# Kernel optimization log

Hardware: AMD Instinct MI355X
Metric: run time of the kernel (lower is better)

Reference implementation:

```python
import jax, jax.numpy as jnp
import numpy as np

D, H, DK = 512, 8, 64
SCALE = 1.5 / 1.0  # gamma/tau, schedule='const'
NEG = -1e30


def _cross(x_q, x_kv, mask_kv, Wq, Wk, Wv, scale):
    # x_q: [B,Tq,D], x_kv: [B,Tk,D], mask_kv: [B,Tk] (1=keep, 0=mask)
    B, Tq, _ = x_q.shape
    Tk = x_kv.shape[1]
    q = (x_q @ Wq.T).reshape(B, Tq, H, DK).transpose(0, 2, 1, 3)
    k = (x_kv @ Wk.T).reshape(B, Tk, H, DK).transpose(0, 2, 1, 3)
    v = (x_kv @ Wv.T).reshape(B, Tk, H, DK).transpose(0, 2, 1, 3)
    logits = jnp.einsum('bhqd,bhkd->bhqk', q, k) * (scale / jnp.sqrt(jnp.float32(DK)))
    if mask_kv is not None:
        logits = jnp.where(mask_kv[:, None, None, :] == 0, NEG, logits)
    attn = jax.nn.softmax(logits, axis=-1)
    out = jnp.einsum('bhqk,bhkd->bhqd', attn, v)
    return out.transpose(0, 2, 1, 3).reshape(B, Tq, D)


def setup_inputs() -> dict:
    key = jax.random.key(0)
    ks = jax.random.split(key, 12)
    B, T = 4, 2048
    inp = {
        'skel_seq': jax.random.normal(ks[0], (B, T, D), jnp.float32),
        'sens_seq': jax.random.normal(ks[1], (B, T, D), jnp.float32),
        'mask_skel': jax.random.randint(ks[2], (B, T), 0, 2, jnp.int32),
        'mask_sens': jax.random.randint(ks[3], (B, T), 0, 2, jnp.int32),
    }
    s = 1.0 / np.sqrt(D)
    names = ['Wq_s2e', 'Wk_e', 'Wv_e', 'Wq_e2s', 'Wk_s', 'Wv_s', 'Wo_s', 'Wo_e']
    for i, n in enumerate(names):
        inp[n] = jax.random.normal(ks[4 + i], (D, D), jnp.float32) * s
    return inp


def reference(skel_seq, sens_seq, mask_skel, mask_sens,
              Wq_s2e, Wk_e, Wv_e, Wq_e2s, Wk_s, Wv_s, Wo_s, Wo_e):
    # skel queries attend over sensor keys/values
    s2e = _cross(skel_seq, sens_seq, mask_sens, Wq_s2e, Wk_e, Wv_e, SCALE) @ Wo_e.T
    # sensor queries attend over skeleton keys/values
    e2s = _cross(sens_seq, skel_seq, mask_skel, Wq_e2s, Wk_s, Wv_s, SCALE) @ Wo_s.T
    return (e2s, s2e)
```

## Files before the change

kernel.cpp:

```cpp
#include <hip/hip_runtime.h>
#include <hip/hip_bf16.h>

#define T_SEQ 2048
#define N_TOK 4194304
#define W_ELEM 262144


typedef float f32x4  __attribute__((ext_vector_type(4)));
typedef short bf16x8 __attribute__((ext_vector_type(8)));

#define SCALE_Q 0.27050532f

__device__ __forceinline__ unsigned short f2b(float f) {
    __hip_bfloat16 h = __float2bfloat16(f);
    return *reinterpret_cast<unsigned short*>(&h);
}

__device__ __forceinline__ int pack2bf(float lo, float hi) {
    return ((int)f2b(hi) << 16) | (int)f2b(lo);
}

__device__ __forceinline__ bf16x8 ldg8(const unsigned short* p) {
    union { int4 i; bf16x8 b; } u;
    u.i = *reinterpret_cast<const int4*>(p);
    return u.b;
}

__device__ __forceinline__ float fexp2(float x) {
#if __has_builtin(__builtin_amdgcn_exp2f)
    return __builtin_amdgcn_exp2f(x);
#else
    return exp2f(x);
#endif
}

typedef unsigned int u32_g __attribute__((address_space(1)));
typedef unsigned int u32_l __attribute__((address_space(3)));
__device__ __forceinline__ void gload_lds16(const void* g, void* l) {
    __builtin_amdgcn_global_load_lds((const u32_g*)g, (u32_l*)l, 16, 0, 0);
}

__device__ __forceinline__ void raw_barrier() {
    __builtin_amdgcn_sched_barrier(0);
    __builtin_amdgcn_s_barrier();
    __builtin_amdgcn_sched_barrier(0);
}

__global__ __launch_bounds__(256)
void prep_bias(const int* __restrict__ ms, const int* __restrict__ mk,
               float* __restrict__ dst)
{
    const int i = (blockIdx.x * 256 + threadIdx.x) * 8;
    const int* m = (i >> 13) ? mk : ms;
    const int rem = i & 8191;
    const int4 a = *reinterpret_cast<const int4*>(&m[rem]);
    const int4 b = *reinterpret_cast<const int4*>(&m[rem + 4]);
    float4 f0, f1;
    f0.x = a.x ? 0.0f : -3e38f; f0.y = a.y ? 0.0f : -3e38f;
    f0.z = a.z ? 0.0f : -3e38f; f0.w = a.w ? 0.0f : -3e38f;
    f1.x = b.x ? 0.0f : -3e38f; f1.y = b.y ? 0.0f : -3e38f;
    f1.z = b.z ? 0.0f : -3e38f; f1.w = b.w ? 0.0f : -3e38f;
    *reinterpret_cast<float4*>(&dst[i])     = f0;
    *reinterpret_cast<float4*>(&dst[i + 4]) = f1;
}

__global__ __launch_bounds__(256)
void to_bf16(const float* __restrict__ s0, const float* __restrict__ s1,
             const float* __restrict__ w0, const float* __restrict__ w1,
             const float* __restrict__ w2, const float* __restrict__ w3,
             const float* __restrict__ w4, const float* __restrict__ w5,
             unsigned short* __restrict__ dst)
{
    const int bid = blockIdx.x;
    int y, x;
    if (bid < 4096) { y = bid >> 11; x = bid & 2047; }
    else { const int t = bid - 4096; y = 2 + (t >> 7); x = t & 127; }
    const float* src;
    size_t off;
    switch (y) {
        case 0: src = s0; off = 0;      break;
        case 1: src = s1; off = N_TOK;  break;
        case 2: src = w0; off = 2 * (size_t)N_TOK;              break;
        case 3: src = w1; off = 2 * (size_t)N_TOK + 1 * W_ELEM; break;
        case 4: src = w2; off = 2 * (size_t)N_TOK + 2 * W_ELEM; break;
        case 5: src = w3; off = 2 * (size_t)N_TOK + 3 * W_ELEM; break;
        case 6: src = w4; off = 2 * (size_t)N_TOK + 4 * W_ELEM; break;
        default: src = w5; off = 2 * (size_t)N_TOK + 5 * W_ELEM; break;
    }
    const int idx = (x * 256 + threadIdx.x) * 8;
    const float4 a = *reinterpret_cast<const float4*>(src + idx);
    const float4 b = *reinterpret_cast<const float4*>(src + idx + 4);
    int4 o;
    o.x = pack2bf(a.x, a.y); o.y = pack2bf(a.z, a.w);
    o.z = pack2bf(b.x, b.y); o.w = pack2bf(b.z, b.w);
    *reinterpret_cast<int4*>(dst + off + idx) = o;
}

#define MF_SETUP                                                               \
    __shared__ short Asm[64][72];                                              \
    __shared__ short Wsm[64][72];                                              \
    const int tid  = threadIdx.x;                                              \
    const int lane = tid & 63;                                                 \
    const int w4   = tid >> 6;                                                 \
    const int nl   = lane & 15;                                                \
    const int quad = lane >> 4;                                                \
    const int n0 = blockIdx.x * 64;                                            \
    const int m0 = blockIdx.y * 64;                                            \
    const int arow = tid >> 2;                                                 \
    const int acol = (tid & 3) * 16;                                           \
    f32x4 acc[4] = {};

#define MF_WRITE_W                                                             \
    {                                                                          \
        int4 x;                                                                \
        x.x = pack2bf(wv[0].x, wv[0].y); x.y = pack2bf(wv[0].z, wv[0].w);      \
        x.z = pack2bf(wv[1].x, wv[1].y); x.w = pack2bf(wv[1].z, wv[1].w);      \
        *reinterpret_cast<int4*>(&Wsm[arow][acol]) = x;                        \
        x.x = pack2bf(wv[2].x, wv[2].y); x.y = pack2bf(wv[2].z, wv[2].w);      \
        x.z = pack2bf(wv[3].x, wv[3].y); x.w = pack2bf(wv[3].z, wv[3].w);      \
        *reinterpret_cast<int4*>(&Wsm[arow][acol + 8]) = x;                    \
    }

#define MF_MMA_LOOP                                                            \
    _Pragma("unroll")                                                          \
    for (int kc = 0; kc < 2; ++kc) {                                           \
        const bf16x8 a = *reinterpret_cast<const bf16x8*>(                     \
            &Asm[w4 * 16 + nl][kc * 32 + quad * 8]);                           \
        _Pragma("unroll")                                                      \
        for (int c = 0; c < 4; ++c) {                                          \
            const bf16x8 bf = *reinterpret_cast<const bf16x8*>(                \
                &Wsm[c * 16 + nl][kc * 32 + quad * 8]);                        \
            acc[c] = __builtin_amdgcn_mfma_f32_16x16x32_bf16(a, bf, acc[c],    \
                                                             0, 0, 0);         \
        }                                                                      \
    }

#define MF_CWRITE_PROJ                                                         \
    if (!trans) {                                                              \
        _Pragma("unroll")                                                      \
        for (int c = 0; c < 4; ++c)                                            \
            _Pragma("unroll")                                                  \
            for (int r = 0; r < 4; ++r)                                        \
                C[(size_t)(m0 + w4 * 16 + quad * 4 + r) * 512 + n0 + c * 16 + nl] = \
                    f2b(acc[c][r] * alpha);                                    \
    } else {                                                                   \
        const int b  = m0 >> 11;                                               \
        const int t0 = (m0 & 2047) + w4 * 16 + quad * 4;                       \
        _Pragma("unroll")                                                      \
        for (int c = 0; c < 4; ++c) {                                          \
            const int n = n0 + c * 16 + nl;                                    \
            ushort4 o;                                                         \
            o.x = f2b(acc[c][0]);                                              \
            o.y = f2b(acc[c][1]);                                              \
            o.z = f2b(acc[c][2]);                                              \
            o.w = f2b(acc[c][3]);                                              \
            *reinterpret_cast<ushort4*>(C + (size_t)(b * 512 + n) * T_SEQ + t0) = o; \
        }                                                                      \
    }

__global__ __launch_bounds__(256)
void proj_all(const float* __restrict__ skel, const float* __restrict__ sens,
              const float* __restrict__ Wq1, const float* __restrict__ Wk1,
              const float* __restrict__ Wv1, const float* __restrict__ Wq2,
              const float* __restrict__ Wk2, const float* __restrict__ Wv2,
              unsigned short* __restrict__ Q1, unsigned short* __restrict__ K1,
              unsigned short* __restrict__ Vt1, unsigned short* __restrict__ Q2,
              unsigned short* __restrict__ K2, unsigned short* __restrict__ Vt2,
              int zbase)
{
    const int z = zbase + blockIdx.z;
    const float* A; const float* W; unsigned short* C;
    float alpha = 1.0f; bool trans = false;
    switch (z) {
        case 0:  A = skel; W = Wq1; C = Q1; alpha = SCALE_Q; break;
        case 1:  A = sens; W = Wk1; C = K1; break;
        case 2:  A = sens; W = Wv1; C = Vt1; trans = true; break;
        case 3:  A = sens; W = Wq2; C = Q2; alpha = SCALE_Q; break;
        case 4:  A = skel; W = Wk2; C = K2; break;
        default: A = skel; W = Wv2; C = Vt2; trans = true; break;
    }

    MF_SETUP
    const float* ap = A + (size_t)(m0 + arow) * 512 + acol;
    const float* wp = W + (size_t)(n0 + arow) * 512 + acol;
    float4 av[4], wv[4];
    #pragma unroll
    for (int j = 0; j < 4; ++j) {
        av[j] = *reinterpret_cast<const float4*>(ap + 4 * j);
        wv[j] = *reinterpret_cast<const float4*>(wp + 4 * j);
    }
    for (int it = 0; it < 8; ++it) {
        __syncthreads();
        {
            int4 x;
            x.x = pack2bf(av[0].x, av[0].y); x.y = pack2bf(av[0].z, av[0].w);
            x.z = pack2bf(av[1].x, av[1].y); x.w = pack2bf(av[1].z, av[1].w);
            *reinterpret_cast<int4*>(&Asm[arow][acol]) = x;
            x.x = pack2bf(av[2].x, av[2].y); x.y = pack2bf(av[2].z, av[2].w);
            x.z = pack2bf(av[3].x, av[3].y); x.w = pack2bf(av[3].z, av[3].w);
            *reinterpret_cast<int4*>(&Asm[arow][acol + 8]) = x;
        }
        MF_WRITE_W
        __syncthreads();
        if (it < 7) {
            const float* apn = ap + (it + 1) * 64;
            const float* wpn = wp + (it + 1) * 64;
            #pragma unroll
            for (int j = 0; j < 4; ++j) {
                av[j] = *reinterpret_cast<const float4*>(apn + 4 * j);
                wv[j] = *reinterpret_cast<const float4*>(wpn + 4 * j);
            }
        }
        MF_MMA_LOOP
    }
    MF_CWRITE_PROJ
}

__global__ __launch_bounds__(256, 3)
void proj_fused(const unsigned short* __restrict__ skb,
                const unsigned short* __restrict__ snb,
                const unsigned short* __restrict__ wball,
                unsigned short* __restrict__ Q1, unsigned short* __restrict__ K1,
                unsigned short* __restrict__ Vt1, unsigned short* __restrict__ Q2,
                unsigned short* __restrict__ K2, unsigned short* __restrict__ Vt2)
{
    __shared__ __align__(16) char smem[49152];
    short (*Al)[128][32] = reinterpret_cast<short (*)[128][32]>(smem);
    short (*Wl)[128][32] = reinterpret_cast<short (*)[128][32]>(smem + 24576);

    const int o   = blockIdx.x;
    const int wg  = (o & 7) * 192 + (o >> 3);
    const int z   = wg >> 8;
    const int idx = wg & 255;
    const int nh  = idx & 3;
    const int mt  = idx >> 2;

    const unsigned short* A = (z == 0 || z >= 4) ? skb : snb;
    const unsigned short* W = wball + (size_t)z * W_ELEM;
    unsigned short* C;
    switch (z) {
        case 0: C = Q1;  break;
        case 1: C = K1;  break;
        case 2: C = Vt1; break;
        case 3: C = Q2;  break;
        case 4: C = K2;  break;
        default: C = Vt2; break;
    }
    const bool trans = (z == 2 || z == 5);
    const float alpha = (z == 0 || z == 3) ? SCALE_Q : 1.0f;

    const int tid  = threadIdx.x;
    const int w    = tid >> 6;
    const int wr   = w >> 1;
    const int wc   = w & 1;
    const int lane = tid & 63;
    const int nl   = lane & 15;
    const int quad = lane >> 4;
    const int rof  = lane >> 2;
    const int cg   = (lane & 3) ^ ((lane >> 3) & 3);

    const int m0g = mt * 128;
    const int n0  = nh * 128;

    const unsigned short* srcA0 = A + (size_t)(m0g + w * 32 + rof) * 512 + cg * 8;
    const unsigned short* srcA1 = srcA0 + (size_t)16 * 512;
    const unsigned short* srcW0 = W + (size_t)(n0 + w * 32 + rof) * 512 + cg * 8;
    const unsigned short* srcW1 = srcW0 + (size_t)16 * 512;

    f32x4 acc[4][4] = {};

    auto stage = [&](int it, int buf) {
        const int k0 = it * 32;
        gload_lds16(srcA0 + k0, &Al[buf][w * 32][0]);
        gload_lds16(srcA1 + k0, &Al[buf][w * 32 + 16][0]);
        gload_lds16(srcW0 + k0, &Wl[buf][w * 32][0]);
        gload_lds16(srcW1 + k0, &Wl[buf][w * 32 + 16][0]);
    };

    stage(0, 0);
    stage(1, 1);
    asm volatile("s_waitcnt vmcnt(4)" ::: "memory");
    raw_barrier();

    const int key = (nl >> 1) & 3;
    int bcur = 0, bpre = 2;
    for (int it = 0; it < 16; ++it) {
        if (it < 14) stage(it + 2, bpre);
        bf16x8 a[4], bb[4];
        #pragma unroll
        for (int am = 0; am < 4; ++am)
            a[am] = *reinterpret_cast<const bf16x8*>(
                &Al[bcur][wr * 64 + am * 16 + nl][(quad ^ key) * 8]);
        #pragma unroll
        for (int bn = 0; bn < 4; ++bn)
            bb[bn] = *reinterpret_cast<const bf16x8*>(
                &Wl[bcur][wc * 64 + bn * 16 + nl][(quad ^ key) * 8]);
        #pragma unroll
        for (int am = 0; am < 4; ++am)
            #pragma unroll
            for (int bn = 0; bn < 4; ++bn)
                acc[am][bn] = __builtin_amdgcn_mfma_f32_16x16x32_bf16(
                    a[am], bb[bn], acc[am][bn], 0, 0, 0);
        if (it < 14)       asm volatile("s_waitcnt vmcnt(4)" ::: "memory");
        else if (it == 14) asm volatile("s_waitcnt vmcnt(0)" ::: "memory");
        raw_barrier();
        bcur = (bcur == 2) ? 0 : bcur + 1;
        bpre = (bpre == 2) ? 0 : bpre + 1;
    }

    if (!trans) {
        short (*Cl)[136] = reinterpret_cast<short (*)[136]>(smem);
        #pragma unroll
        for (int am = 0; am < 4; ++am)
            #pragma unroll
            for (int bn = 0; bn < 4; ++bn)
                #pragma unroll
                for (int r = 0; r < 4; ++r)
                    Cl[wr * 64 + am * 16 + quad * 4 + r][wc * 64 + bn * 16 + nl] =
                        (short)f2b(acc[am][bn][r] * alpha);
        __syncthreads();
        const int lr = tid >> 1;
        const int ch = (tid & 1) * 64;
        unsigned short* cp = C + (size_t)(m0g + lr) * 512 + n0 + ch;
        #pragma unroll
        for (int j = 0; j < 8; ++j)
            *reinterpret_cast<int4*>(cp + j * 8) =
                *reinterpret_cast<const int4*>(&Cl[lr][ch + j * 8]);
    } else {
        short (*Tl)[136] = reinterpret_cast<short (*)[136]>(smem);
        #pragma unroll
        for (int am = 0; am < 4; ++am)
            #pragma unroll
            for (int bn = 0; bn < 4; ++bn) {
                int* dst = reinterpret_cast<int*>(
                    &Tl[wc * 64 + bn * 16 + nl][wr * 64 + am * 16 + quad * 4]);
                dst[0] = pack2bf(acc[am][bn][0], acc[am][bn][1]);
                dst[1] = pack2bf(acc[am][bn][2], acc[am][bn][3]);
            }
        __syncthreads();
        const int bq = m0g >> 11;
        const int t0 = m0g & 2047;
        const int nr = tid >> 1;
        const int tc = (tid & 1) * 64;
        unsigned short* vp = C + (size_t)(bq * 512 + n0 + nr) * T_SEQ + t0 + tc;
        #pragma unroll
        for (int j = 0; j < 8; ++j)
            *reinterpret_cast<int4*>(vp + j * 8) =
                *reinterpret_cast<const int4*>(&Tl[nr][tc + j * 8]);
    }
}

__global__ __launch_bounds__(256, 2)
void out_fused(const unsigned short* __restrict__ AO1, const float* __restrict__ Wo1,
               float* __restrict__ C1,
               const unsigned short* __restrict__ AO2, const float* __restrict__ Wo2,
               float* __restrict__ C2)
{
    __shared__ __align__(16) char smem[67584];
    short (*Al)[128][64] = reinterpret_cast<short (*)[128][64]>(smem);
    short (*Wl)[128][64] = reinterpret_cast<short (*)[128][64]>(smem + 32768);

    const int o   = blockIdx.x;
    const int wg  = (o & 7) * 64 + (o >> 3);
    const int z   = wg >> 8;
    const int idx = wg & 255;
    const int nh  = idx & 3;
    const int mt  = idx >> 2;

    const unsigned short* A = z ? AO2 : AO1;
    const float* W = z ? Wo2 : Wo1;
    float* C = z ? C2 : C1;

    const int tid  = threadIdx.x;
    const int w    = tid >> 6;
    const int wr   = w >> 1;
    const int wc   = w & 1;
    const int lane = tid & 63;
    const int nl   = lane & 15;
    const int quad = lane >> 4;
    const int r8   = lane >> 3;
    const int cg   = (lane & 7) ^ r8;

    const int m0g = mt * 128;
    const int n0  = nh * 128;

    const unsigned short* Ab = A + (size_t)m0g * 512 + cg * 8;

    const int rw_ = tid >> 1;
    const int ch_ = (tid & 1) * 32;
    const int key = rw_ & 7;

    f32x4 acc[4][4] = {};
    float4 wreg[8];

    auto stageA = [&](int it, int buf) {
        const int k0 = it * 64;
        #pragma unroll
        for (int g = 0; g < 4; ++g) {
            const int rr = w * 32 + g * 8;
            gload_lds16(Ab + (size_t)(rr + r8) * 512 + k0, &Al[buf][rr][0]);
        }
    };
    auto wload = [&](int it) {
        const float* wp = W + (size_t)(n0 + rw_) * 512 + it * 64 + ch_;
        #pragma unroll
        for (int j = 0; j < 8; ++j)
            wreg[j] = *reinterpret_cast<const float4*>(wp + 4 * j);
    };
    auto wstore = [&](int buf) {
        #pragma unroll
        for (int j = 0; j < 8; ++j) {
            int2 pk;
            pk.x = pack2bf(wreg[j].x, wreg[j].y);
            pk.y = pack2bf(wreg[j].z, wreg[j].w);
            const int slot = ((tid & 1) * 4 + (j >> 1)) ^ key;
            *reinterpret_cast<int2*>(
                &Wl[buf][rw_][slot * 8 + (j & 1) * 4]) = pk;
        }
    };

    wload(0);
    stageA(0, 0);
    asm volatile("s_waitcnt vmcnt(0)" ::: "memory");
    wstore(0);
    __syncthreads();

    const int sw = nl & 7;
    for (int it = 0; it < 8; ++it) {
        const int buf = it & 1;
        if (it < 7) { stageA(it + 1, buf ^ 1); wload(it + 1); }
        #pragma unroll
        for (int kc = 0; kc < 2; ++kc) {
            bf16x8 a[4], bb[4];
            #pragma unroll
            for (int am = 0; am < 4; ++am)
                a[am] = *reinterpret_cast<const bf16x8*>(
                    &Al[buf][wr * 64 + am * 16 + nl][((kc * 4 + quad) ^ sw) * 8]);
            #pragma unroll
            for (int bn = 0; bn < 4; ++bn)
                bb[bn] = *reinterpret_cast<const bf16x8*>(
                    &Wl[buf][wc * 64 + bn * 16 + nl][((kc * 4 + quad) ^ sw) * 8]);
            #pragma unroll
            for (int am = 0; am < 4; ++am)
                #pragma unroll
                for (int bn = 0; bn < 4; ++bn)
                    acc[am][bn] = __builtin_amdgcn_mfma_f32_16x16x32_bf16(
                        a[am], bb[bn], acc[am][bn], 0, 0, 0);
        }
        asm volatile("s_waitcnt vmcnt(0)" ::: "memory");
        if (it < 7) wstore(buf ^ 1);
        __syncthreads();
    }

    float (*Cl)[132] = reinterpret_cast<float (*)[132]>(smem);
    #pragma unroll
    for (int am = 0; am < 4; ++am)
        #pragma unroll
        for (int bn = 0; bn < 4; ++bn)
            #pragma unroll
            for (int r = 0; r < 4; ++r)
                Cl[wr * 64 + am * 16 + quad * 4 + r][wc * 64 + bn * 16 + nl] =
                    acc[am][bn][r];
    __syncthreads();
    const int lr = tid >> 1;
    const int fc = (tid & 1) * 64;
    float* cp = C + (size_t)(m0g + lr) * 512 + n0 + fc;
    #pragma unroll
    for (int j = 0; j < 16; ++j)
        *reinterpret_cast<float4*>(cp + j * 4) =
            *reinterpret_cast<const float4*>(&Cl[lr][fc + j * 4]);
}

__global__ __launch_bounds__(256)
void out_proj(const unsigned short* __restrict__ AO1, const float* __restrict__ Wo1,
              float* __restrict__ C1,
              const unsigned short* __restrict__ AO2, const float* __restrict__ Wo2,
              float* __restrict__ C2, int zbase)
{
    const int z = zbase + blockIdx.z;
    const unsigned short* A = z ? AO2 : AO1;
    const float* W = z ? Wo2 : Wo1;
    float* C = z ? C2 : C1;

    MF_SETUP
    const unsigned short* ap = A + (size_t)(m0 + arow) * 512 + acol;
    const float* wp = W + (size_t)(n0 + arow) * 512 + acol;
    int4 ai[2];
    float4 wv[4];
    ai[0] = *reinterpret_cast<const int4*>(ap);
    ai[1] = *reinterpret_cast<const int4*>(ap + 8);
    #pragma unroll
    for (int j = 0; j < 4; ++j)
        wv[j] = *reinterpret_cast<const float4*>(wp + 4 * j);
    for (int it = 0; it < 8; ++it) {
        __syncthreads();
        *reinterpret_cast<int4*>(&Asm[arow][acol])     = ai[0];
        *reinterpret_cast<int4*>(&Asm[arow][acol + 8]) = ai[1];
        MF_WRITE_W
        __syncthreads();
        if (it < 7) {
            const unsigned short* apn = ap + (it + 1) * 64;
            const float* wpn = wp + (it + 1) * 64;
            ai[0] = *reinterpret_cast<const int4*>(apn);
            ai[1] = *reinterpret_cast<const int4*>(apn + 8);
            #pragma unroll
            for (int j = 0; j < 4; ++j)
                wv[j] = *reinterpret_cast<const float4*>(wpn + 4 * j);
        }
        MF_MMA_LOOP
    }
    #pragma unroll
    for (int c = 0; c < 4; ++c)
        #pragma unroll
        for (int r = 0; r < 4; ++r)
            C[(size_t)(m0 + w4 * 16 + quad * 4 + r) * 512 + n0 + c * 16 + nl] =
                acc[c][r];
}

__global__ __launch_bounds__(512)
void attn_mfma(const unsigned short* Q1x, const unsigned short* __restrict__ K1x,
               const unsigned short* __restrict__ V1x, const float* __restrict__ b1x,
               unsigned short* AO1x,
               const unsigned short* Q2x, const unsigned short* __restrict__ K2x,
               const unsigned short* __restrict__ V2x, const float* __restrict__ b2x,
               unsigned short* AO2x)
{
    __shared__ short Kl[2][64][64];
    __shared__ short Vl[2][64][64];
    __shared__ short Pl[8][16][64];

    const int dir = blockIdx.y >> 5;
    const unsigned short* Q  = dir ? Q2x : Q1x;
    const unsigned short* K  = dir ? K2x : K1x;
    const unsigned short* Vt = dir ? V2x : V1x;
    const float* biasD       = dir ? b2x : b1x;
    unsigned short* AO       = dir ? AO2x : AO1x;

    const int tid  = threadIdx.x;
    const int w    = tid >> 6;
    const int lane = tid & 63;
    const int nl   = lane & 15;
    const int quad = lane >> 4;
    const int qt = blockIdx.x;
    const int bh = blockIdx.y & 31;
    const int b = bh >> 3, h = bh & 7;
    const size_t tb = (size_t)b * (T_SEQ * 512);
    const float* biasB = biasD + b * T_SEQ;

    const int r8 = lane >> 3;
    const int cg = (lane & 7) ^ r8;
    const int sr = w * 8;

    const unsigned short* qp = Q + tb + (size_t)(qt * 128 + w * 16 + nl) * 512 + h * 64 + quad * 8;
    const bf16x8 qb0 = ldg8(qp);
    const bf16x8 qb1 = ldg8(qp + 32);

    float l_run = 0.0f;
    f32x4 o[4] = {};

    gload_lds16(K  + tb + (size_t)(sr + r8) * 512 + h * 64 + cg * 8, &Kl[0][sr][0]);
    gload_lds16(Vt + (size_t)(b * 512 + h * 64 + sr + r8) * T_SEQ + cg * 8, &Vl[0][sr][0]);
    asm volatile("s_waitcnt vmcnt(0)" ::: "memory");
    __syncthreads();

    const int swz = nl & 7;

    for (int kt = 0; kt < 32; ++kt) {
        const int cur = kt & 1;
        short (*Kb)[64] = Kl[cur];
        short (*Vb)[64] = Vl[cur];

        if (kt < 31) {
            short (*Kn)[64] = Kl[cur ^ 1];
            short (*Vn)[64] = Vl[cur ^ 1];
            gload_lds16(K  + tb + (size_t)((kt + 1) * 64 + sr + r8) * 512 + h * 64 + cg * 8, &Kn[sr][0]);
            gload_lds16(Vt + (size_t)(b * 512 + h * 64 + sr + r8) * T_SEQ + (size_t)(kt + 1) * 64 + cg * 8, &Vn[sr][0]);
        }

        float p[4][4];
        #pragma unroll
        for (int s = 0; s < 4; ++s) {
            const bf16x8 k0 = *reinterpret_cast<const bf16x8*>(&Kb[s * 16 + nl][(quad ^ swz) * 8]);
            const bf16x8 k1 = *reinterpret_cast<const bf16x8*>(&Kb[s * 16 + nl][((4 + quad) ^ swz) * 8]);
            const float4 bb = *reinterpret_cast<const float4*>(
                &biasB[kt * 64 + s * 16 + quad * 4]);
            f32x4 z = {bb.x, bb.y, bb.z, bb.w};
            z = __builtin_amdgcn_mfma_f32_16x16x32_bf16(k0, qb0, z, 0, 0, 0);
            z = __builtin_amdgcn_mfma_f32_16x16x32_bf16(k1, qb1, z, 0, 0, 0);
            p[s][0] = fexp2(z[0]);
            p[s][1] = fexp2(z[1]);
            p[s][2] = fexp2(z[2]);
            p[s][3] = fexp2(z[3]);
            l_run += p[s][0] + p[s][1] + p[s][2] + p[s][3];
        }

        #pragma unroll
        for (int s = 0; s < 4; ++s) {
            int2 pk;
            pk.x = pack2bf(p[s][0], p[s][1]);
            pk.y = pack2bf(p[s][2], p[s][3]);
            const int slot = (2 * s + (quad >> 1)) ^ swz;
            *reinterpret_cast<int2*>(&Pl[w][nl][slot * 8 + (quad & 1) * 4]) = pk;
        }

        const bf16x8 pa0 = *reinterpret_cast<const bf16x8*>(&Pl[w][nl][(quad ^ swz) * 8]);
        const bf16x8 pa1 = *reinterpret_cast<const bf16x8*>(&Pl[w][nl][((4 + quad) ^ swz) * 8]);
        __builtin_amdgcn_s_setprio(1);
        #pragma unroll
        for (int sd = 0; sd < 4; ++sd) {
            const bf16x8 v0 = *reinterpret_cast<const bf16x8*>(&Vb[sd * 16 + nl][(quad ^ swz) * 8]);
            const bf16x8 v1 = *reinterpret_cast<const bf16x8*>(&Vb[sd * 16 + nl][((4 + quad) ^ swz) * 8]);
            o[sd] = __builtin_amdgcn_mfma_f32_16x16x32_bf16(v0, pa0, o[sd], 0, 0, 0);
            o[sd] = __builtin_amdgcn_mfma_f32_16x16x32_bf16(v1, pa1, o[sd], 0, 0, 0);
        }
        __builtin_amdgcn_s_setprio(0);

        asm volatile("s_waitcnt vmcnt(0)" ::: "memory");
        __syncthreads();
    }

    l_run += __shfl_xor(l_run, 16);
    l_run += __shfl_xor(l_run, 32);
    const float inv = 1.0f / l_run;
    unsigned short* ob = AO + tb + (size_t)(qt * 128 + w * 16 + nl) * 512 + h * 64 + quad * 4;
    #pragma unroll
    for (int sd = 0; sd < 4; ++sd) {
        ushort4 o4;
        o4.x = f2b(o[sd][0] * inv);
        o4.y = f2b(o[sd][1] * inv);
        o4.z = f2b(o[sd][2] * inv);
        o4.w = f2b(o[sd][3] * inv);
        *reinterpret_cast<ushort4*>(ob + sd * 16) = o4;
    }
}

extern "C" void kernel_launch(void* const* d_in, const int* in_sizes, int n_in,
                              void* d_out, int out_size, void* d_ws, size_t ws_size,
                              hipStream_t stream) {
    const float* skel = (const float*)d_in[0];
    const float* sens = (const float*)d_in[1];
    const int* mask_skel = (const int*)d_in[2];
    const int* mask_sens = (const int*)d_in[3];
    const float* Wq_s2e = (const float*)d_in[4];
    const float* Wk_e   = (const float*)d_in[5];
    const float* Wv_e   = (const float*)d_in[6];
    const float* Wq_e2s = (const float*)d_in[7];
    const float* Wk_s   = (const float*)d_in[8];
    const float* Wv_s   = (const float*)d_in[9];
    const float* Wo_s   = (const float*)d_in[10];
    const float* Wo_e   = (const float*)d_in[11];
    float* out = (float*)d_out;

    unsigned short* Q1 = (unsigned short*)d_ws;
    unsigned short* K1 = Q1 + N_TOK;
    unsigned short* V1 = K1 + N_TOK;

    const bool big = ws_size >= (size_t)6 * N_TOK * sizeof(unsigned short);

    if (big) {
        unsigned short* Q2 = V1 + N_TOK;
        unsigned short* K2 = Q2 + N_TOK;
        unsigned short* V2 = K2 + N_TOK;
        unsigned short* SC  = (unsigned short*)d_out;
        unsigned short* skb = SC;
        unsigned short* snb = SC + N_TOK;
        unsigned short* wb  = SC + 2 * (size_t)N_TOK;
        float* biasS = (float*)(SC + 2 * (size_t)N_TOK + 6 * W_ELEM);
        float* bias0 = biasS;
        float* bias1 = biasS + 4 * T_SEQ;
        prep_bias<<<dim3(8), 256, 0, stream>>>(mask_sens, mask_skel, biasS);
        to_bf16<<<dim3(4864), 256, 0, stream>>>(
            skel, sens, Wq_s2e, Wk_e, Wv_e, Wq_e2s, Wk_s, Wv_s, SC);
        proj_fused<<<dim3(1536), 256, 0, stream>>>(
            skb, snb, wb, Q1, K1, V1, Q2, K2, V2);
        attn_mfma<<<dim3(16, 64), 512, 0, stream>>>(
            Q1, K1, V1, bias0, Q1,
            Q2, K2, V2, bias1, Q2);
        out_fused<<<dim3(512), 256, 0, stream>>>(
            Q1, Wo_e, out + N_TOK, Q2, Wo_s, out);
    } else {
        float* bias0 = out;
        float* bias1 = out + 8192;
        prep_bias<<<dim3(8), 256, 0, stream>>>(mask_sens, mask_skel, bias0);
        proj_all<<<dim3(8, 128, 3), 256, 0, stream>>>(
            skel, sens, Wq_s2e, Wk_e, Wv_e, Wq_e2s, Wk_s, Wv_s,
            Q1, K1, V1, Q1, K1, V1, 0);
        attn_mfma<<<dim3(16, 32), 512, 0, stream>>>(
            Q1, K1, V1, bias0, Q1, Q1, K1, V1, bias0, Q1);
        out_proj<<<dim3(8, 128, 1), 256, 0, stream>>>(
            Q1, Wo_e, out + N_TOK, Q1, Wo_s, out, 0);
        proj_all<<<dim3(8, 128, 3), 256, 0, stream>>>(
            skel, sens, Wq_s2e, Wk_e, Wv_e, Wq_e2s, Wk_s, Wv_s,
            Q1, K1, V1, Q1, K1, V1, 3);
        attn_mfma<<<dim3(16, 32), 512, 0, stream>>>(
            Q1, K1, V1, bias1, Q1, Q1, K1, V1, bias1, Q1);
        out_proj<<<dim3(8, 128, 1), 256, 0, stream>>>(
            Q1, Wo_s, out, Q1, Wo_s, out, 1);
    }
}
```

Measured before the change: 283.9 us.

## Triple-buffer attention and out-projection loads, pre-convert Wo to bf16

```diff
diff --git a/kernel.cpp b/kernel.cpp
--- a/kernel.cpp
+++ b/kernel.cpp
@@ -94,6 +94,21 @@
     o.x = pack2bf(a.x, a.y); o.y = pack2bf(a.z, a.w);
     o.z = pack2bf(b.x, b.y); o.w = pack2bf(b.z, b.w);
     *reinterpret_cast<int4*>(dst + off + idx) = o;
+}
+
+__global__ __launch_bounds__(256)
+void wo_bf16(const float* __restrict__ we, const float* __restrict__ wsrc,
+             unsigned short* __restrict__ dst)
+{
+    const int i = (blockIdx.x * 256 + threadIdx.x) * 8;
+    const float* src = (i >= W_ELEM) ? wsrc : we;
+    const int rem = i & (W_ELEM - 1);
+    const float4 a = *reinterpret_cast<const float4*>(src + rem);
+    const float4 b = *reinterpret_cast<const float4*>(src + rem + 4);
+    int4 o;
+    o.x = pack2bf(a.x, a.y); o.y = pack2bf(a.z, a.w);
+    o.z = pack2bf(b.x, b.y); o.w = pack2bf(b.z, b.w);
+    *reinterpret_cast<int4*>(dst + i) = o;
 }
 
 #define MF_SETUP                                                               \
@@ -350,15 +365,15 @@
     }
 }
 
-__global__ __launch_bounds__(256, 2)
-void out_fused(const unsigned short* __restrict__ AO1, const float* __restrict__ Wo1,
-               float* __restrict__ C1,
-               const unsigned short* __restrict__ AO2, const float* __restrict__ Wo2,
-               float* __restrict__ C2)
+__global__ __launch_bounds__(256, 3)
+void out_fused(const unsigned short* __restrict__ AO1,
+               const unsigned short* __restrict__ Wb1, float* __restrict__ C1,
+               const unsigned short* __restrict__ AO2,
+               const unsigned short* __restrict__ Wb2, float* __restrict__ C2)
 {
-    __shared__ __align__(16) char smem[67584];
-    short (*Al)[128][64] = reinterpret_cast<short (*)[128][64]>(smem);
-    short (*Wl)[128][64] = reinterpret_cast<short (*)[128][64]>(smem + 32768);
+    __shared__ __align__(16) char smem[49152];
+    short (*Al)[128][32] = reinterpret_cast<short (*)[128][32]>(smem);
+    short (*Wl)[128][32] = reinterpret_cast<short (*)[128][32]>(smem + 24576);
 
     const int o   = blockIdx.x;
     const int wg  = (o & 7) * 64 + (o >> 3);
@@ -368,7 +383,7 @@
     const int mt  = idx >> 2;
 
     const unsigned short* A = z ? AO2 : AO1;
-    const float* W = z ? Wo2 : Wo1;
+    const unsigned short* W = z ? Wb2 : Wb1;
     float* C = z ? C2 : C1;
 
     const int tid  = threadIdx.x;
@@ -378,97 +393,98 @@
     const int lane = tid & 63;
     const int nl   = lane & 15;
     const int quad = lane >> 4;
-    const int r8   = lane >> 3;
-    const int cg   = (lane & 7) ^ r8;
+    const int rof  = lane >> 2;
+    const int cg   = (lane & 3) ^ ((lane >> 3) & 3);
 
     const int m0g = mt * 128;
     const int n0  = nh * 128;
 
-    const unsigned short* Ab = A + (size_t)m0g * 512 + cg * 8;
-
-    const int rw_ = tid >> 1;
-    const int ch_ = (tid & 1) * 32;
-    const int key = rw_ & 7;
+    const unsigned short* srcA0 = A + (size_t)(m0g + w * 32 + rof) * 512 + cg * 8;
+    const unsigned short* srcA1 = srcA0 + (size_t)16 * 512;
+    const unsigned short* srcW0 = W + (size_t)(n0 + w * 32 + rof) * 512 + cg * 8;
+    const unsigned short* srcW1 = srcW0 + (size_t)16 * 512;
 
     f32x4 acc[4][4] = {};
-    float4 wreg[8];
-
-    auto stageA = [&](int it, int buf) {
-        const int k0 = it * 64;
-        #pragma unroll
-        for (int g = 0; g < 4; ++g) {
-            const int rr = w * 32 + g * 8;
-            gload_lds16(Ab + (size_t)(rr + r8) * 512 + k0, &Al[buf][rr][0]);
-        }
+
+    auto stage = [&](int it, int buf) {
+        const int k0 = it * 32;
+        gload_lds16(srcA0 + k0, &Al[buf][w * 32][0]);
+        gload_lds16(srcA1 + k0, &Al[buf][w * 32 + 16][0]);
+        gload_lds16(srcW0 + k0, &Wl[buf][w * 32][0]);
+        gload_lds16(srcW1 + k0, &Wl[buf][w * 32 + 16][0]);
     };
-    auto wload = [&](int it) {
-        const float* wp = W + (size_t)(n0 + rw_) * 512 + it * 64 + ch_;
-        #pragma unroll
-        for (int j = 0; j < 8; ++j)
-            wreg[j] = *reinterpret_cast<const float4*>(wp + 4 * j);
-    };
-    auto wstore = [&](int buf) {
-        #pragma unroll
-        for (int j = 0; j < 8; ++j) {
-            int2 pk;
-            pk.x = pack2bf(wreg[j].x, wreg[j].y);
-            pk.y = pack2bf(wreg[j].z, wreg[j].w);
-            const int slot = ((tid & 1) * 4 + (j >> 1)) ^ key;
-            *reinterpret_cast<int2*>(
-                &Wl[buf][rw_][slot * 8 + (j & 1) * 4]) = pk;
-        }
-    };
-
-    wload(0);
-    stageA(0, 0);
-    asm volatile("s_waitcnt vmcnt(0)" ::: "memory");
-    wstore(0);
-    __syncthreads();
-
-    const int sw = nl & 7;
-    for (int it = 0; it < 8; ++it) {
-        const int buf = it & 1;
-        if (it < 7) { stageA(it + 1, buf ^ 1); wload(it + 1); }
-        #pragma unroll
-        for (int kc = 0; kc < 2; ++kc) {
-            bf16x8 a[4], bb[4];
-            #pragma unroll
-            for (int am = 0; am < 4; ++am)
-                a[am] = *reinterpret_cast<const bf16x8*>(
-                    &Al[buf][wr * 64 + am * 16 + nl][((kc * 4 + quad) ^ sw) * 8]);
+
+    stage(0, 0);
+    stage(1, 1);
+    asm volatile("s_waitcnt vmcnt(4)" ::: "memory");
+    raw_barrier();
+
+    const int key = (nl >> 1) & 3;
+    int bcur = 0, bpre = 2;
+    for (int it = 0; it < 16; ++it) {
+        if (it < 14) stage(it + 2, bpre);
+        bf16x8 a[4], bb[4];
+        #pragma unroll
+        for (int am = 0; am < 4; ++am)
+            a[am] = *reinterpret_cast<const bf16x8*>(
+                &Al[bcur][wr * 64 + am * 16 + nl][(quad ^ key) * 8]);
+        #pragma unroll
+        for (int bn = 0; bn < 4; ++bn)
+            bb[bn] = *reinterpret_cast<const bf16x8*>(
+                &Wl[bcur][wc * 64 + bn * 16 + nl][(quad ^ key) * 8]);
+        #pragma unroll
+        for (int am = 0; am < 4; ++am)
             #pragma unroll
             for (int bn = 0; bn < 4; ++bn)
-                bb[bn] = *reinterpret_cast<const bf16x8*>(
-                    &Wl[buf][wc * 64 + bn * 16 + nl][((kc * 4 + quad) ^ sw) * 8]);
+                acc[am][bn] = __builtin_amdgcn_mfma_f32_16x16x32_bf16(
+                    a[am], bb[bn], acc[am][bn], 0, 0, 0);
+        if (it < 14)       asm volatile("s_waitcnt vmcnt(4)" ::: "memory");
+        else if (it == 14) asm volatile("s_waitcnt vmcnt(0)" ::: "memory");
+        raw_barrier();
+        bcur = (bcur == 2) ? 0 : bcur + 1;
+        bpre = (bpre == 2) ? 0 : bpre + 1;
+    }
+
+    float (*Cl)[132] = reinterpret_cast<float (*)[132]>(smem);
+    const int lr = tid >> 2;
+    const int fc = (tid & 3) * 32;
+    if (wr == 0) {
+        #pragma unroll
+        for (int am = 0; am < 4; ++am)
             #pragma unroll
-            for (int am = 0; am < 4; ++am)
+            for (int bn = 0; bn < 4; ++bn)
                 #pragma unroll
-                for (int bn = 0; bn < 4; ++bn)
-                    acc[am][bn] = __builtin_amdgcn_mfma_f32_16x16x32_bf16(
-                        a[am], bb[bn], acc[am][bn], 0, 0, 0);
-        }
-        asm volatile("s_waitcnt vmcnt(0)" ::: "memory");
-        if (it < 7) wstore(buf ^ 1);
-        __syncthreads();
-    }
-
-    float (*Cl)[132] = reinterpret_cast<float (*)[132]>(smem);
-    #pragma unroll
-    for (int am = 0; am < 4; ++am)
-        #pragma unroll
-        for (int bn = 0; bn < 4; ++bn)
+                for (int r = 0; r < 4; ++r)
+                    Cl[am * 16 + quad * 4 + r][wc * 64 + bn * 16 + nl] =
+                        acc[am][bn][r];
+    }
+    __syncthreads();
+    {
+        float* cp = C + (size_t)(m0g + lr) * 512 + n0 + fc;
+        #pragma unroll
+        for (int j = 0; j < 8; ++j)
+            *reinterpret_cast<float4*>(cp + j * 4) =
+                *reinterpret_cast<const float4*>(&Cl[lr][fc + j * 4]);
+    }
+    __syncthreads();
+    if (wr == 1) {
+        #pragma unroll
+        for (int am = 0; am < 4; ++am)
             #pragma unroll
-            for (int r = 0; r < 4; ++r)
-                Cl[wr * 64 + am * 16 + quad * 4 + r][wc * 64 + bn * 16 + nl] =
-                    acc[am][bn][r];
+            for (int bn = 0; bn < 4; ++bn)
+                #pragma unroll
+                for (int r = 0; r < 4; ++r)
+                    Cl[am * 16 + quad * 4 + r][wc * 64 + bn * 16 + nl] =
+                        acc[am][bn][r];
+    }
     __syncthreads();
-    const int lr = tid >> 1;
-    const int fc = (tid & 1) * 64;
-    float* cp = C + (size_t)(m0g + lr) * 512 + n0 + fc;
-    #pragma unroll
-    for (int j = 0; j < 16; ++j)
-        *reinterpret_cast<float4*>(cp + j * 4) =
-            *reinterpret_cast<const float4*>(&Cl[lr][fc + j * 4]);
+    {
+        float* cp = C + (size_t)(m0g + 64 + lr) * 512 + n0 + fc;
+        #pragma unroll
+        for (int j = 0; j < 8; ++j)
+            *reinterpret_cast<float4*>(cp + j * 4) =
+                *reinterpret_cast<const float4*>(&Cl[lr][fc + j * 4]);
+    }
 }
 
 __global__ __launch_bounds__(256)
@@ -525,8 +541,8 @@
                const unsigned short* __restrict__ V2x, const float* __restrict__ b2x,
                unsigned short* AO2x)
 {
-    __shared__ short Kl[2][64][64];
-    __shared__ short Vl[2][64][64];
+    __shared__ short Kl[3][64][64];
+    __shared__ short Vl[3][64][64];
     __shared__ short Pl[8][16][64];
 
     const int dir = blockIdx.y >> 5;
@@ -551,6 +567,14 @@
     const int cg = (lane & 7) ^ r8;
     const int sr = w * 8;
 
+    auto stageKV = [&](int t, int buf) {
+        gload_lds16(K + tb + (size_t)(t * 64 + sr + r8) * 512 + h * 64 + cg * 8,
+                    &Kl[buf][sr][0]);
+        gload_lds16(Vt + (size_t)(b * 512 + h * 64 + sr + r8) * T_SEQ +
+                        (size_t)t * 64 + cg * 8,
+                    &Vl[buf][sr][0]);
+    };
+
     const unsigned short* qp = Q + tb + (size_t)(qt * 128 + w * 16 + nl) * 512 + h * 64 + quad * 8;
     const bf16x8 qb0 = ldg8(qp);
     const bf16x8 qb1 = ldg8(qp + 32);
@@ -558,24 +582,18 @@
     float l_run = 0.0f;
     f32x4 o[4] = {};
 
-    gload_lds16(K  + tb + (size_t)(sr + r8) * 512 + h * 64 + cg * 8, &Kl[0][sr][0]);
-    gload_lds16(Vt + (size_t)(b * 512 + h * 64 + sr + r8) * T_SEQ + cg * 8, &Vl[0][sr][0]);
-    asm volatile("s_waitcnt vmcnt(0)" ::: "memory");
-    __syncthreads();
+    stageKV(0, 0);
+    stageKV(1, 1);
+    asm volatile("s_waitcnt vmcnt(2)" ::: "memory");
+    raw_barrier();
 
     const int swz = nl & 7;
 
+    int bcur = 0, bpre = 2;
     for (int kt = 0; kt < 32; ++kt) {
-        const int cur = kt & 1;
-        short (*Kb)[64] = Kl[cur];
-        short (*Vb)[64] = Vl[cur];
-
-        if (kt < 31) {
-            short (*Kn)[64] = Kl[cur ^ 1];
-            short (*Vn)[64] = Vl[cur ^ 1];
-            gload_lds16(K  + tb + (size_t)((kt + 1) * 64 + sr + r8) * 512 + h * 64 + cg * 8, &Kn[sr][0]);
-            gload_lds16(Vt + (size_t)(b * 512 + h * 64 + sr + r8) * T_SEQ + (size_t)(kt + 1) * 64 + cg * 8, &Vn[sr][0]);
-        }
+        if (kt < 30) stageKV(kt + 2, bpre);
+        short (*Kb)[64] = Kl[bcur];
+        short (*Vb)[64] = Vl[bcur];
 
         float p[4][4];
         #pragma unroll
@@ -615,8 +633,11 @@
         }
         __builtin_amdgcn_s_setprio(0);
 
-        asm volatile("s_waitcnt vmcnt(0)" ::: "memory");
-        __syncthreads();
+        if (kt < 30)       asm volatile("s_waitcnt vmcnt(2)" ::: "memory");
+        else if (kt == 30) asm volatile("s_waitcnt vmcnt(0)" ::: "memory");
+        if (kt < 31) raw_barrier();
+        bcur = (bcur == 2) ? 0 : bcur + 1;
+        bpre = (bpre == 2) ? 0 : bpre + 1;
     }
 
     l_run += __shfl_xor(l_run, 16);
@@ -676,8 +697,9 @@
         attn_mfma<<<dim3(16, 64), 512, 0, stream>>>(
             Q1, K1, V1, bias0, Q1,
             Q2, K2, V2, bias1, Q2);
+        wo_bf16<<<dim3(256), 256, 0, stream>>>(Wo_e, Wo_s, K1);
         out_fused<<<dim3(512), 256, 0, stream>>>(
-            Q1, Wo_e, out + N_TOK, Q2, Wo_s, out);
+            Q1, K1, out + N_TOK, Q2, K1 + W_ELEM, out);
     } else {
         float* bias0 = out;
         float* bias1 = out + 8192;
```

New measurement: 273.6 us. 3.6% less time.
